# Kernel optimization log

Hardware: AMD Instinct MI355X
Metric: run time of the kernel (lower is better)

Reference implementation:

```python
import jax, jax.numpy as jnp
import numpy as np

GAMMA = 0.1
IN_FEATURES = 256 * 2048  # flattened per-sample size
K = int(GAMMA * IN_FEATURES)  # 52428


def setup_inputs() -> dict:
    key = jax.random.key(0)
    x = jax.random.normal(key, (64, 256, 2048), dtype=jnp.float32)
    return {"x": x}


def reference(x) -> jnp.ndarray:
    # Flatten each sample: [B, D1*D2]
    b = x.shape[0]
    tmpx = x.reshape(b, -1)
    # k-th largest value per row (torch.topk returns sorted descending; [:, -1] is k-th largest)
    topval = jax.lax.top_k(tmpx, K)[0][:, -1]  # [B]
    topval = topval.reshape(-1, 1, 1)  # broadcast over [B, D1, D2]
    # Faithful to original: mask keeps values strictly BELOW the threshold (topval > x)
    out = jnp.where(topval > x, x, jnp.zeros((), dtype=x.dtype))
    return out
```

## Files before the change

### kernel.cpp

```cpp
#include <hip/hip_runtime.h>
#include <stdint.h>

constexpr int ROWS = 64;
constexpr int D = 1 << 19;
constexpr uint32_t KSEL = 52428;
constexpr int HBPR = 16;
constexpr int HCHUNK = D / HBPR;
constexpr int MBPR = 32;
constexpr int MCHUNK = D / MBPR;
constexpr uint32_t CAND_MAX = 12288;
constexpr int LBUF = 1024;

constexpr size_t OFF_BH   = 0;
constexpr size_t OFF_CNT  = 2097152;
constexpr size_t OFF_SEL  = OFF_CNT + 64;
constexpr size_t OFF_RANK = OFF_SEL + 64;
constexpr size_t OFF_CAND = OFF_RANK + 64;

typedef float f32x4 __attribute__((ext_vector_type(4)));

__device__ __forceinline__ uint32_t mono(uint32_t f) {
    uint32_t m = (uint32_t)((int32_t)f >> 31) | 0x80000000u;
    return f ^ m;
}

__global__ __launch_bounds__(256) void hist_pass(const uint32_t* __restrict__ x,
                                                 uint32_t* __restrict__ ws) {
    __shared__ uint32_t lh[4096];
    for (int i = threadIdx.x; i < 4096; i += 256) lh[i] = 0;
    __syncthreads();
    const int bid = blockIdx.x;
    const int row = bid / HBPR, chunk = bid % HBPR;
    const uint4* p = (const uint4*)(x + (size_t)row * D + (size_t)chunk * HCHUNK);
    for (int i = threadIdx.x; i < HCHUNK / 4; i += 256) {
        uint4 v = p[i];
        atomicAdd(&lh[mono(v.x) >> 20], 1u);
        atomicAdd(&lh[mono(v.y) >> 20], 1u);
        atomicAdd(&lh[mono(v.z) >> 20], 1u);
        atomicAdd(&lh[mono(v.w) >> 20], 1u);
    }
    __syncthreads();
    uint32_t* bh = ws + OFF_BH + (size_t)bid * 2048;
    for (int i = threadIdx.x; i < 2048; i += 256)
        bh[i] = (lh[2 * i] & 0xFFFFu) | (lh[2 * i + 1] << 16);
}

__global__ __launch_bounds__(256) void reduce_select(uint32_t* __restrict__ ws) {
    constexpr int PER = 16;
    __shared__ uint32_t sc[256];
    const int row = blockIdx.x, t = threadIdx.x;
    const int base_bin = 4080 - PER * t;
    uint32_t acc[PER];
#pragma unroll
    for (int j = 0; j < PER; ++j) acc[j] = 0;
    for (int c = 0; c < HBPR; ++c) {
        const uint32_t* src = ws + OFF_BH + ((size_t)row * HBPR + c) * 2048 + base_bin / 2;
#pragma unroll
        for (int w = 0; w < PER / 2; ++w) {
            uint32_t pk = src[w];
            acc[2 * w] += pk & 0xFFFFu;
            acc[2 * w + 1] += pk >> 16;
        }
    }
    uint32_t s = 0;
#pragma unroll
    for (int j = 0; j < PER; ++j) s += acc[j];
    sc[t] = s;
    __syncthreads();
    for (int off = 1; off < 256; off <<= 1) {
        uint32_t v = (t >= off) ? sc[t - off] : 0u;
        __syncthreads();
        sc[t] += v;
        __syncthreads();
    }
    uint32_t excl = sc[t] - s;
    if (excl < KSEL && excl + s >= KSEL) {
        uint32_t c = excl;
        for (int j = PER - 1; j >= 0; --j) {
            c += acc[j];
            if (c >= KSEL) {
                ws[OFF_SEL + row] = (uint32_t)(base_bin + j);
                ws[OFF_RANK + row] = KSEL - (c - acc[j]);
                break;
            }
        }
    }
    if (t == 0) ws[OFF_CNT + row] = 0;
}

__global__ __launch_bounds__(256) void mask_compact(const uint32_t* __restrict__ x,
                                                    float* __restrict__ out,
                                                    uint32_t* __restrict__ ws) {
    __shared__ uint32_t lkey[LBUF];
    __shared__ uint32_t lidx[LBUF];
    __shared__ uint32_t ln, gbase;
    if (threadIdx.x == 0) ln = 0;
    __syncthreads();
    const int row = blockIdx.x / MBPR, chunk = blockIdx.x % MBPR, t = threadIdx.x;
    const uint32_t b = ws[OFF_SEL + row];
    const uint4* p = (const uint4*)(x + (size_t)row * D + (size_t)chunk * MCHUNK);
    f32x4* o = (f32x4*)(out + (size_t)row * D + (size_t)chunk * MCHUNK);
    for (int i = t; i < MCHUNK / 4; i += 256) {
        uint4 v = p[i];
        f32x4 ov;
        uint32_t idx0 = (uint32_t)chunk * MCHUNK + (uint32_t)i * 4;
#define PROC(comp, lane_j)                                                 \
        {                                                                  \
            uint32_t u = mono(comp);                                       \
            uint32_t bu = u >> 20;                                         \
            ov[lane_j] = (bu > b) ? 0.0f : __uint_as_float(comp);          \
            if (bu == b) {                                                 \
                uint32_t s = atomicAdd(&ln, 1u);                           \
                if (s < (uint32_t)LBUF) { lkey[s] = u; lidx[s] = idx0 + lane_j; } \
            }                                                              \
        }
        PROC(v.x, 0)
        PROC(v.y, 1)
        PROC(v.z, 2)
        PROC(v.w, 3)
#undef PROC
        __builtin_nontemporal_store(ov, &o[i]);
    }
    __syncthreads();
    uint32_t m = ln < (uint32_t)LBUF ? ln : (uint32_t)LBUF;
    if (t == 0) gbase = atomicAdd(&ws[OFF_CNT + row], m);
    __syncthreads();
    uint32_t base = gbase;
    uint2* cp = (uint2*)(ws + OFF_CAND) + (size_t)row * CAND_MAX;
    for (uint32_t i = t; i < m; i += 256) {
        uint32_t slot = base + i;
        if (slot < CAND_MAX) cp[slot] = make_uint2(lkey[i], lidx[i]);
    }
}

__global__ __launch_bounds__(256) void select_fix(float* __restrict__ out,
                                                  uint32_t* __restrict__ ws) {
    __shared__ uint32_t ckey[CAND_MAX];
    __shared__ uint32_t h[1024];
    __shared__ uint32_t sc[256];
    __shared__ uint32_t bcast[2];
    const int row = blockIdx.x, t = threadIdx.x;
    uint32_t n = ws[OFF_CNT + row];
    if (n > CAND_MAX) n = CAND_MAX;
    const uint2* cp = (const uint2*)(ws + OFF_CAND) + (size_t)row * CAND_MAX;
    uint32_t k = ws[OFF_RANK + row];
    uint32_t b = ws[OFF_SEL + row];

    for (uint32_t i = t; i < n; i += 256) ckey[i] = cp[i].x;

    for (int i = t; i < 1024; i += 256) h[i] = 0;
    __syncthreads();
    for (uint32_t i = t; i < n; i += 256) atomicAdd(&h[(ckey[i] >> 10) & 0x3FFu], 1u);
    __syncthreads();
    {
        int hi = 1023 - t * 4;
        uint32_t s = 0;
        for (int j = 0; j < 4; ++j) s += h[hi - j];
        sc[t] = s;
        __syncthreads();
        for (int off = 1; off < 256; off <<= 1) {
            uint32_t v = (t >= off) ? sc[t - off] : 0u;
            __syncthreads();
            sc[t] += v;
            __syncthreads();
        }
        uint32_t excl = sc[t] - s;
        if (excl < k && excl + s >= k) {
            uint32_t cc = excl;
            for (int j = 0; j < 4; ++j) {
                int bin = hi - j;
                uint32_t hb = h[bin];
                cc += hb;
                if (cc >= k) { bcast[0] = (uint32_t)bin; bcast[1] = k - (cc - hb); break; }
            }
        }
    }
    __syncthreads();
    uint32_t b1 = bcast[0], k2 = bcast[1];
    __syncthreads();

    for (int i = t; i < 1024; i += 256) h[i] = 0;
    __syncthreads();
    for (uint32_t i = t; i < n; i += 256) {
        uint32_t u = ckey[i];
        if (((u >> 10) & 0x3FFu) == b1) atomicAdd(&h[u & 0x3FFu], 1u);
    }
    __syncthreads();
    {
        int hi = 1023 - t * 4;
        uint32_t s = 0;
        for (int j = 0; j < 4; ++j) s += h[hi - j];
        sc[t] = s;
        __syncthreads();
        for (int off = 1; off < 256; off <<= 1) {
            uint32_t v = (t >= off) ? sc[t - off] : 0u;
            __syncthreads();
            sc[t] += v;
            __syncthreads();
        }
        uint32_t excl = sc[t] - s;
        if (excl < k2 && excl + s >= k2) {
            uint32_t cc = excl;
            for (int j = 0; j < 4; ++j) {
                int bin = hi - j;
                uint32_t hb = h[bin];
                cc += hb;
                if (cc >= k2) {
                    bcast[0] = (b << 20) | (b1 << 10) | (uint32_t)bin;
                    break;
                }
            }
        }
    }
    __syncthreads();
    uint32_t thr_key = bcast[0];

    float* orow = out + (size_t)row * D;
    for (uint32_t i = t; i < n; i += 256) {
        uint2 pr = cp[i];
        if (pr.x >= thr_key) orow[pr.y] = 0.0f;
    }
}

extern "C" void kernel_launch(void* const* d_in, const int* in_sizes, int n_in,
                              void* d_out, int out_size, void* d_ws, size_t ws_size,
                              hipStream_t stream) {
    (void)in_sizes; (void)n_in; (void)out_size; (void)ws_size;
    const uint32_t* xu = (const uint32_t*)d_in[0];
    float* outp = (float*)d_out;
    uint32_t* ws = (uint32_t*)d_ws;

    hist_pass<<<ROWS * HBPR, 256, 0, stream>>>(xu, ws);
    reduce_select<<<ROWS, 256, 0, stream>>>(ws);
    mask_compact<<<ROWS * MBPR, 256, 0, stream>>>(xu, outp, ws);
    select_fix<<<ROWS, 256, 0, stream>>>(outp, ws);
}
```

Baseline: 110.4 us.

## Speculate threshold bucket to drop histogram pass, with exact fallback path

```diff
diff --git a/kernel.cpp b/kernel.cpp
--- a/kernel.cpp
+++ b/kernel.cpp
@@ -4,18 +4,15 @@
 constexpr int ROWS = 64;
 constexpr int D = 1 << 19;
 constexpr uint32_t KSEL = 52428;
-constexpr int HBPR = 16;
-constexpr int HCHUNK = D / HBPR;
 constexpr int MBPR = 32;
 constexpr int MCHUNK = D / MBPR;
-constexpr uint32_t CAND_MAX = 12288;
-constexpr int LBUF = 1024;
-
-constexpr size_t OFF_BH   = 0;
-constexpr size_t OFF_CNT  = 2097152;
-constexpr size_t OFF_SEL  = OFF_CNT + 64;
-constexpr size_t OFF_RANK = OFF_SEL + 64;
-constexpr size_t OFF_CAND = OFF_RANK + 64;
+constexpr int LBUF = 896;
+constexpr uint32_t PRED_B = 0xBFAu;
+constexpr uint32_t NCAND_MAX = 12288;
+
+constexpr size_t OFF_SCNT = 0;
+constexpr size_t OFF_ACNT = 2048;
+constexpr size_t OFF_PAIR = 4096;
 
 typedef float f32x4 __attribute__((ext_vector_type(4)));
 
@@ -24,82 +21,20 @@
     return f ^ m;
 }
 
-__global__ __launch_bounds__(256) void hist_pass(const uint32_t* __restrict__ x,
+__global__ __launch_bounds__(256) void mask_pred(const uint32_t* __restrict__ x,
+                                                 float* __restrict__ out,
                                                  uint32_t* __restrict__ ws) {
-    __shared__ uint32_t lh[4096];
-    for (int i = threadIdx.x; i < 4096; i += 256) lh[i] = 0;
-    __syncthreads();
-    const int bid = blockIdx.x;
-    const int row = bid / HBPR, chunk = bid % HBPR;
-    const uint4* p = (const uint4*)(x + (size_t)row * D + (size_t)chunk * HCHUNK);
-    for (int i = threadIdx.x; i < HCHUNK / 4; i += 256) {
-        uint4 v = p[i];
-        atomicAdd(&lh[mono(v.x) >> 20], 1u);
-        atomicAdd(&lh[mono(v.y) >> 20], 1u);
-        atomicAdd(&lh[mono(v.z) >> 20], 1u);
-        atomicAdd(&lh[mono(v.w) >> 20], 1u);
-    }
-    __syncthreads();
-    uint32_t* bh = ws + OFF_BH + (size_t)bid * 2048;
-    for (int i = threadIdx.x; i < 2048; i += 256)
-        bh[i] = (lh[2 * i] & 0xFFFFu) | (lh[2 * i + 1] << 16);
-}
-
-__global__ __launch_bounds__(256) void reduce_select(uint32_t* __restrict__ ws) {
-    constexpr int PER = 16;
-    __shared__ uint32_t sc[256];
-    const int row = blockIdx.x, t = threadIdx.x;
-    const int base_bin = 4080 - PER * t;
-    uint32_t acc[PER];
-#pragma unroll
-    for (int j = 0; j < PER; ++j) acc[j] = 0;
-    for (int c = 0; c < HBPR; ++c) {
-        const uint32_t* src = ws + OFF_BH + ((size_t)row * HBPR + c) * 2048 + base_bin / 2;
-#pragma unroll
-        for (int w = 0; w < PER / 2; ++w) {
-            uint32_t pk = src[w];
-            acc[2 * w] += pk & 0xFFFFu;
-            acc[2 * w + 1] += pk >> 16;
-        }
-    }
-    uint32_t s = 0;
-#pragma unroll
-    for (int j = 0; j < PER; ++j) s += acc[j];
-    sc[t] = s;
-    __syncthreads();
-    for (int off = 1; off < 256; off <<= 1) {
-        uint32_t v = (t >= off) ? sc[t - off] : 0u;
-        __syncthreads();
-        sc[t] += v;
-        __syncthreads();
-    }
-    uint32_t excl = sc[t] - s;
-    if (excl < KSEL && excl + s >= KSEL) {
-        uint32_t c = excl;
-        for (int j = PER - 1; j >= 0; --j) {
-            c += acc[j];
-            if (c >= KSEL) {
-                ws[OFF_SEL + row] = (uint32_t)(base_bin + j);
-                ws[OFF_RANK + row] = KSEL - (c - acc[j]);
-                break;
-            }
-        }
-    }
-    if (t == 0) ws[OFF_CNT + row] = 0;
-}
-
-__global__ __launch_bounds__(256) void mask_compact(const uint32_t* __restrict__ x,
-                                                    float* __restrict__ out,
-                                                    uint32_t* __restrict__ ws) {
     __shared__ uint32_t lkey[LBUF];
     __shared__ uint32_t lidx[LBUF];
-    __shared__ uint32_t ln, gbase;
+    __shared__ uint32_t red[256];
+    __shared__ uint32_t ln;
     if (threadIdx.x == 0) ln = 0;
     __syncthreads();
-    const int row = blockIdx.x / MBPR, chunk = blockIdx.x % MBPR, t = threadIdx.x;
-    const uint32_t b = ws[OFF_SEL + row];
+    const int bid = blockIdx.x;
+    const int row = bid / MBPR, chunk = bid % MBPR, t = threadIdx.x;
     const uint4* p = (const uint4*)(x + (size_t)row * D + (size_t)chunk * MCHUNK);
     f32x4* o = (f32x4*)(out + (size_t)row * D + (size_t)chunk * MCHUNK);
+    uint32_t above = 0;
     for (int i = t; i < MCHUNK / 4; i += 256) {
         uint4 v = p[i];
         f32x4 ov;
@@ -108,8 +43,9 @@
         {                                                                  \
             uint32_t u = mono(comp);                                       \
             uint32_t bu = u >> 20;                                         \
-            ov[lane_j] = (bu > b) ? 0.0f : __uint_as_float(comp);          \
-            if (bu == b) {                                                 \
+            ov[lane_j] = (bu > PRED_B) ? 0.0f : __uint_as_float(comp);     \
+            above += (bu > PRED_B);                                        \
+            if (bu == PRED_B) {                                            \
                 uint32_t s = atomicAdd(&ln, 1u);                           \
                 if (s < (uint32_t)LBUF) { lkey[s] = u; lidx[s] = idx0 + lane_j; } \
             }                                                              \
@@ -121,36 +57,186 @@
 #undef PROC
         __builtin_nontemporal_store(ov, &o[i]);
     }
-    __syncthreads();
+    red[t] = above;
+    __syncthreads();
+    for (int off = 128; off > 0; off >>= 1) {
+        if (t < off) red[t] += red[t + off];
+        __syncthreads();
+    }
+    if (t == 0) {
+        ws[OFF_SCNT + bid] = ln;
+        ws[OFF_ACNT + bid] = red[0];
+    }
     uint32_t m = ln < (uint32_t)LBUF ? ln : (uint32_t)LBUF;
-    if (t == 0) gbase = atomicAdd(&ws[OFF_CNT + row], m);
-    __syncthreads();
-    uint32_t base = gbase;
-    uint2* cp = (uint2*)(ws + OFF_CAND) + (size_t)row * CAND_MAX;
+    uint32_t* sk = ws + OFF_PAIR + (size_t)bid * (2 * LBUF);
     for (uint32_t i = t; i < m; i += 256) {
-        uint32_t slot = base + i;
-        if (slot < CAND_MAX) cp[slot] = make_uint2(lkey[i], lidx[i]);
+        sk[i] = lkey[i];
+        sk[LBUF + i] = lidx[i];
     }
 }
 
-__global__ __launch_bounds__(256) void select_fix(float* __restrict__ out,
-                                                  uint32_t* __restrict__ ws) {
-    __shared__ uint32_t ckey[CAND_MAX];
+__global__ __launch_bounds__(256) void finalize(const uint32_t* __restrict__ x,
+                                                float* __restrict__ out,
+                                                uint32_t* __restrict__ ws) {
+    __shared__ uint32_t ckey[NCAND_MAX];
     __shared__ uint32_t h[1024];
     __shared__ uint32_t sc[256];
-    __shared__ uint32_t bcast[2];
+    __shared__ uint32_t soff[MBPR + 1];
+    __shared__ uint32_t bc[3];
     const int row = blockIdx.x, t = threadIdx.x;
-    uint32_t n = ws[OFF_CNT + row];
-    if (n > CAND_MAX) n = CAND_MAX;
-    const uint2* cp = (const uint2*)(ws + OFF_CAND) + (size_t)row * CAND_MAX;
-    uint32_t k = ws[OFF_RANK + row];
-    uint32_t b = ws[OFF_SEL + row];
-
-    for (uint32_t i = t; i < n; i += 256) ckey[i] = cp[i].x;
+
+    if (t == 0) {
+        uint32_t acc = 0, mx = 0, ab = 0;
+        for (int s = 0; s < MBPR; ++s) {
+            uint32_t c = ws[OFF_SCNT + (size_t)row * MBPR + s];
+            uint32_t a = ws[OFF_ACNT + (size_t)row * MBPR + s];
+            soff[s] = acc;
+            if (c > mx) mx = c;
+            acc += c;
+            ab += a;
+        }
+        soff[MBPR] = acc;
+        bc[0] = acc;
+        bc[1] = ab;
+        bc[2] = (mx <= (uint32_t)LBUF && acc <= NCAND_MAX &&
+                 ab < KSEL && ab + acc >= KSEL) ? 1u : 0u;
+    }
+    __syncthreads();
+    const uint32_t n = bc[0], above = bc[1], valid = bc[2];
+
+    if (valid) {
+        const uint32_t k = KSEL - above;
+        for (int s = 0; s < MBPR; ++s) {
+            uint32_t cnt = soff[s + 1] - soff[s];
+            const uint32_t* sk = ws + OFF_PAIR + ((size_t)row * MBPR + s) * (2 * LBUF);
+            for (uint32_t i = t; i < cnt; i += 256) ckey[soff[s] + i] = sk[i];
+        }
+        for (int i = t; i < 1024; i += 256) h[i] = 0;
+        __syncthreads();
+        for (uint32_t i = t; i < n; i += 256) atomicAdd(&h[(ckey[i] >> 10) & 0x3FFu], 1u);
+        __syncthreads();
+        {
+            int hi = 1023 - t * 4;
+            uint32_t s = 0;
+            for (int j = 0; j < 4; ++j) s += h[hi - j];
+            sc[t] = s;
+            __syncthreads();
+            for (int off = 1; off < 256; off <<= 1) {
+                uint32_t v = (t >= off) ? sc[t - off] : 0u;
+                __syncthreads();
+                sc[t] += v;
+                __syncthreads();
+            }
+            uint32_t excl = sc[t] - s;
+            if (excl < k && excl + s >= k) {
+                uint32_t cc = excl;
+                for (int j = 0; j < 4; ++j) {
+                    int bin = hi - j;
+                    uint32_t hb = h[bin];
+                    cc += hb;
+                    if (cc >= k) { bc[0] = (uint32_t)bin; bc[1] = k - (cc - hb); break; }
+                }
+            }
+        }
+        __syncthreads();
+        uint32_t b1 = bc[0], k2 = bc[1];
+        __syncthreads();
+        for (int i = t; i < 1024; i += 256) h[i] = 0;
+        __syncthreads();
+        for (uint32_t i = t; i < n; i += 256) {
+            uint32_t u = ckey[i];
+            if (((u >> 10) & 0x3FFu) == b1) atomicAdd(&h[u & 0x3FFu], 1u);
+        }
+        __syncthreads();
+        {
+            int hi = 1023 - t * 4;
+            uint32_t s = 0;
+            for (int j = 0; j < 4; ++j) s += h[hi - j];
+            sc[t] = s;
+            __syncthreads();
+            for (int off = 1; off < 256; off <<= 1) {
+                uint32_t v = (t >= off) ? sc[t - off] : 0u;
+                __syncthreads();
+                sc[t] += v;
+                __syncthreads();
+            }
+            uint32_t excl = sc[t] - s;
+            if (excl < k2 && excl + s >= k2) {
+                uint32_t cc = excl;
+                for (int j = 0; j < 4; ++j) {
+                    int bin = hi - j;
+                    uint32_t hb = h[bin];
+                    cc += hb;
+                    if (cc >= k2) {
+                        bc[0] = (PRED_B << 20) | (b1 << 10) | (uint32_t)bin;
+                        break;
+                    }
+                }
+            }
+        }
+        __syncthreads();
+        const uint32_t thr_key = bc[0];
+        float* orow = out + (size_t)row * D;
+        for (int s = 0; s < MBPR; ++s) {
+            uint32_t cnt = soff[s + 1] - soff[s];
+            const uint32_t* sk = ws + OFF_PAIR + ((size_t)row * MBPR + s) * (2 * LBUF);
+            for (uint32_t i = t; i < cnt; i += 256) {
+                if (sk[i] >= thr_key) orow[sk[LBUF + i]] = 0.0f;
+            }
+        }
+        return;
+    }
+
+    const uint4* px = (const uint4*)(x + (size_t)row * D);
+    uint32_t* h4k = ckey;
+
+    for (int i = t; i < 4096; i += 256) h4k[i] = 0;
+    __syncthreads();
+    for (int i = t; i < D / 4; i += 256) {
+        uint4 v = px[i];
+        atomicAdd(&h4k[mono(v.x) >> 20], 1u);
+        atomicAdd(&h4k[mono(v.y) >> 20], 1u);
+        atomicAdd(&h4k[mono(v.z) >> 20], 1u);
+        atomicAdd(&h4k[mono(v.w) >> 20], 1u);
+    }
+    __syncthreads();
+    {
+        int hi = 4095 - t * 16;
+        uint32_t loc[16];
+        uint32_t s = 0;
+#pragma unroll
+        for (int j = 0; j < 16; ++j) { loc[j] = h4k[hi - j]; s += loc[j]; }
+        sc[t] = s;
+        __syncthreads();
+        for (int off = 1; off < 256; off <<= 1) {
+            uint32_t v = (t >= off) ? sc[t - off] : 0u;
+            __syncthreads();
+            sc[t] += v;
+            __syncthreads();
+        }
+        uint32_t excl = sc[t] - s;
+        if (excl < KSEL && excl + s >= KSEL) {
+            uint32_t c = excl;
+            for (int j = 0; j < 16; ++j) {
+                c += loc[j];
+                if (c >= KSEL) { bc[0] = (uint32_t)(hi - j); bc[1] = KSEL - (c - loc[j]); break; }
+            }
+        }
+    }
+    __syncthreads();
+    const uint32_t B = bc[0], r1 = bc[1];
+    __syncthreads();
 
     for (int i = t; i < 1024; i += 256) h[i] = 0;
     __syncthreads();
-    for (uint32_t i = t; i < n; i += 256) atomicAdd(&h[(ckey[i] >> 10) & 0x3FFu], 1u);
+    for (int i = t; i < D / 4; i += 256) {
+        uint4 v = px[i];
+        uint32_t u;
+        u = mono(v.x); if ((u >> 20) == B) atomicAdd(&h[(u >> 10) & 0x3FFu], 1u);
+        u = mono(v.y); if ((u >> 20) == B) atomicAdd(&h[(u >> 10) & 0x3FFu], 1u);
+        u = mono(v.z); if ((u >> 20) == B) atomicAdd(&h[(u >> 10) & 0x3FFu], 1u);
+        u = mono(v.w); if ((u >> 20) == B) atomicAdd(&h[(u >> 10) & 0x3FFu], 1u);
+    }
     __syncthreads();
     {
         int hi = 1023 - t * 4;
@@ -165,25 +251,30 @@
             __syncthreads();
         }
         uint32_t excl = sc[t] - s;
-        if (excl < k && excl + s >= k) {
+        if (excl < r1 && excl + s >= r1) {
             uint32_t cc = excl;
             for (int j = 0; j < 4; ++j) {
                 int bin = hi - j;
                 uint32_t hb = h[bin];
                 cc += hb;
-                if (cc >= k) { bcast[0] = (uint32_t)bin; bcast[1] = k - (cc - hb); break; }
-            }
-        }
-    }
-    __syncthreads();
-    uint32_t b1 = bcast[0], k2 = bcast[1];
+                if (cc >= r1) { bc[0] = (uint32_t)bin; bc[1] = r1 - (cc - hb); break; }
+            }
+        }
+    }
+    __syncthreads();
+    const uint32_t pref22 = (B << 10) | bc[0];
+    const uint32_t r2 = bc[1];
     __syncthreads();
 
     for (int i = t; i < 1024; i += 256) h[i] = 0;
     __syncthreads();
-    for (uint32_t i = t; i < n; i += 256) {
-        uint32_t u = ckey[i];
-        if (((u >> 10) & 0x3FFu) == b1) atomicAdd(&h[u & 0x3FFu], 1u);
+    for (int i = t; i < D / 4; i += 256) {
+        uint4 v = px[i];
+        uint32_t u;
+        u = mono(v.x); if ((u >> 10) == pref22) atomicAdd(&h[u & 0x3FFu], 1u);
+        u = mono(v.y); if ((u >> 10) == pref22) atomicAdd(&h[u & 0x3FFu], 1u);
+        u = mono(v.z); if ((u >> 10) == pref22) atomicAdd(&h[u & 0x3FFu], 1u);
+        u = mono(v.w); if ((u >> 10) == pref22) atomicAdd(&h[u & 0x3FFu], 1u);
     }
     __syncthreads();
     {
@@ -199,26 +290,28 @@
             __syncthreads();
         }
         uint32_t excl = sc[t] - s;
-        if (excl < k2 && excl + s >= k2) {
+        if (excl < r2 && excl + s >= r2) {
             uint32_t cc = excl;
             for (int j = 0; j < 4; ++j) {
                 int bin = hi - j;
                 uint32_t hb = h[bin];
                 cc += hb;
-                if (cc >= k2) {
-                    bcast[0] = (b << 20) | (b1 << 10) | (uint32_t)bin;
-                    break;
-                }
-            }
-        }
-    }
-    __syncthreads();
-    uint32_t thr_key = bcast[0];
-
-    float* orow = out + (size_t)row * D;
-    for (uint32_t i = t; i < n; i += 256) {
-        uint2 pr = cp[i];
-        if (pr.x >= thr_key) orow[pr.y] = 0.0f;
+                if (cc >= r2) { bc[0] = (pref22 << 10) | (uint32_t)bin; break; }
+            }
+        }
+    }
+    __syncthreads();
+    const uint32_t thr_key = bc[0];
+
+    f32x4* of = (f32x4*)(out + (size_t)row * D);
+    for (int i = t; i < D / 4; i += 256) {
+        uint4 v = px[i];
+        f32x4 ov;
+        ov[0] = (mono(v.x) < thr_key) ? __uint_as_float(v.x) : 0.0f;
+        ov[1] = (mono(v.y) < thr_key) ? __uint_as_float(v.y) : 0.0f;
+        ov[2] = (mono(v.z) < thr_key) ? __uint_as_float(v.z) : 0.0f;
+        ov[3] = (mono(v.w) < thr_key) ? __uint_as_float(v.w) : 0.0f;
+        __builtin_nontemporal_store(ov, &of[i]);
     }
 }
 
@@ -230,8 +323,6 @@
     float* outp = (float*)d_out;
     uint32_t* ws = (uint32_t*)d_ws;
 
-    hist_pass<<<ROWS * HBPR, 256, 0, stream>>>(xu, ws);
-    reduce_select<<<ROWS, 256, 0, stream>>>(ws);
-    mask_compact<<<ROWS * MBPR, 256, 0, stream>>>(xu, outp, ws);
-    select_fix<<<ROWS, 256, 0, stream>>>(outp, ws);
+    mask_pred<<<ROWS * MBPR, 256, 0, stream>>>(xu, outp, ws);
+    finalize<<<ROWS, 256, 0, stream>>>(xu, outp, ws);
 }
```

Result: slower. 116.6 us (+5.6%).
